# Performance work log

Hardware: AMD Instinct MI355X
Metric: run time of the kernel (lower is better)

Reference implementation:

```python
import jax, jax.numpy as jnp
import numpy as np

V = 100000   # vocab (input_size == output_size)
H = 300      # glove_embed_dim == hidden_size
L = 64       # max_length
B = 64       # batch_size


def gru_step(x, h, W_ih, W_hh, b_ih, b_hh):
    # PyTorch nn.GRU single step. x,h: [B,H]; W_*: [3H,H]; b_*: [3H]
    gi = x @ W_ih.T + b_ih
    gh = h @ W_hh.T + b_hh
    i_r, i_z, i_n = jnp.split(gi, 3, axis=-1)
    h_r, h_z, h_n = jnp.split(gh, 3, axis=-1)
    r = jax.nn.sigmoid(i_r + h_r)
    z = jax.nn.sigmoid(i_z + h_z)
    n = jnp.tanh(i_n + r * h_n)
    return (1.0 - z) * n + z * h


def setup_inputs() -> dict:
    key = jax.random.key(0)
    ks = jax.random.split(key, 12)
    s = 1.0 / np.sqrt(H)
    u = lambda k, shape: jax.random.uniform(k, shape, jnp.float32, -s, s)
    return {
        "input": jax.random.randint(ks[0], (L, B), 0, V),
        "emb": jax.random.normal(ks[1], (V, H), jnp.float32),
        "enc_W_ih": u(ks[2], (3 * H, H)), "enc_W_hh": u(ks[3], (3 * H, H)),
        "enc_b_ih": u(ks[4], (3 * H,)), "enc_b_hh": u(ks[5], (3 * H,)),
        "dec_W_ih": u(ks[6], (3 * H, H)), "dec_W_hh": u(ks[7], (3 * H, H)),
        "dec_b_ih": u(ks[8], (3 * H,)), "dec_b_hh": u(ks[9], (3 * H,)),
        "out_W": u(ks[10], (V, H)), "out_b": u(ks[11], (V,)),
    }


def reference(input, emb, enc_W_ih, enc_W_hh, enc_b_ih, enc_b_hh,
              dec_W_ih, dec_W_hh, dec_b_ih, dec_b_hh, out_W, out_b):
    max_len, batch = input.shape

    # ---- encoder: GRU over token embeddings ----
    def enc_step(h, ids):
        x = emb[ids]  # [B,H]
        h_new = gru_step(x, h, enc_W_ih, enc_W_hh, enc_b_ih, enc_b_hh)
        return h_new, None

    h0 = jnp.zeros((batch, H), jnp.float32)
    enc_h, _ = jax.lax.scan(enc_step, h0, input)

    # ---- decoder: greedy generation for max_len steps ----
    def dec_step(carry, _):
        h, ids = carry
        x = jax.nn.relu(emb[ids])
        h_new = gru_step(x, h, dec_W_ih, dec_W_hh, dec_b_ih, dec_b_hh)
        logp = jax.nn.log_softmax(h_new @ out_W.T + out_b, axis=1)  # [B,V]
        new_ids = jnp.argmax(logp, axis=1)  # topk(1)
        return (h_new, new_ids), new_ids.astype(jnp.float32)

    init_ids = jnp.zeros((batch,), jnp.int64 if input.dtype == jnp.int64 else jnp.int32)
    _, out = jax.lax.scan(dec_step, (enc_h, init_ids), None, length=max_len)
    return out  # [max_len, batch] float token ids
```

## Files before the change

kernel.cpp:

```cpp
#include <hip/hip_runtime.h>

#define HD 300
#define KC 75
#define BD 64
#define VD 100000
#define LD 64
#define NM32 3126
#define NT16 6252
#define MARGIN 0.05f

typedef unsigned long long u64;
typedef short short8 __attribute__((ext_vector_type(8)));
typedef float f32x4 __attribute__((ext_vector_type(4)));

__device__ __forceinline__ float sigm(float x) { return 1.0f / (1.0f + expf(-x)); }

__device__ __forceinline__ int tidx(int k, int b) {
  return (k >> 2) * 256 + b * 4 + (k & 3);
}

__device__ __forceinline__ unsigned enc32(float f) {
  unsigned u = __float_as_uint(f);
  return (u & 0x80000000u) ? ~u : (u | 0x80000000u);
}
__device__ __forceinline__ float dec32(unsigned e) {
  unsigned u = (e & 0x80000000u) ? (e & 0x7FFFFFFFu) : ~e;
  return __uint_as_float(u);
}
__device__ __forceinline__ unsigned short f2bf(float f) {
  unsigned u = __float_as_uint(f);
  unsigned r = u + 0x7FFFu + ((u >> 16) & 1u);
  return (unsigned short)(r >> 16);
}
__device__ __forceinline__ u64 shfl64(u64 v, int m) {
  int lo = __shfl_xor((int)(unsigned)v, m, 64);
  int hi = __shfl_xor((int)(unsigned)(v >> 32), m, 64);
  return ((u64)(unsigned)hi << 32) | (unsigned)lo;
}
__device__ __forceinline__ u64 umax64(u64 a, u64 b) { return a > b ? a : b; }
__device__ __forceinline__ void top2(u64 k, u64& b, u64& r) {
  if (k > b) { r = b; b = k; } else if (k > r) r = k;
}

__global__ __launch_bounds__(320) void k_prep(
    const int* __restrict__ input, const float* __restrict__ emb,
    float* __restrict__ xall)
{
  const int t = blockIdx.x, b = blockIdx.y;
  const int k = threadIdx.x;
  if (k >= HD) return;
  const int id = input[t * BD + b];
  xall[t * (KC * 256) + tidx(k, b)] = emb[(size_t)id * HD + k];
}

__global__ __launch_bounds__(320) void k_init(
    float* __restrict__ hT, const float* __restrict__ emb, float* __restrict__ xdec,
    unsigned* __restrict__ hbp)
{
  const int b = blockIdx.x;
  const int k = threadIdx.x;
  const int gi = b * 320 + k;
  if (gi < 10240) hbp[gi] = 0u;
  if (k >= HD) return;
  hT[tidx(k, b)] = 0.f;
  xdec[tidx(k, b)] = fmaxf(emb[k], 0.f);
}

template <bool PACK>
__global__ __launch_bounds__(768) void k_gru(
    const float* __restrict__ xT, const float* __restrict__ hT_in,
    const float* __restrict__ W_ih, const float* __restrict__ W_hh,
    const float* __restrict__ b_ih, const float* __restrict__ b_hh,
    float* __restrict__ hT_out, unsigned* __restrict__ hbp)
{
  const int w = __builtin_amdgcn_readfirstlane(threadIdx.x >> 6);
  const int b = threadIdx.x & 63;
  const int half = (w >= 6) ? 1 : 0;
  const int ww = w - 6 * half;
  const int m = ww & 1;
  const int g = ww >> 1;
  const int i0 = blockIdx.x * 4;

  const float* src = m ? hT_in : xT;
  const float* M   = m ? W_hh : W_ih;
  const float* row0 = M + (size_t)(g * HD + i0) * HD;

  float4 a0 = {0,0,0,0}, a1 = {0,0,0,0}, a2 = {0,0,0,0}, a3 = {0,0,0,0};

  const int kcB = half ? 38 : 0;
  const int kcE = half ? KC : 38;
  for (int kc = kcB; kc < kcE; kc++) {
    const float4 s = *(const float4*)(src + kc * 256 + b * 4);
    const float4 w0 = *(const float4*)(row0 + kc * 4);
    const float4 w1 = *(const float4*)(row0 + HD + kc * 4);
    const float4 w2 = *(const float4*)(row0 + 2 * HD + kc * 4);
    const float4 w3 = *(const float4*)(row0 + 3 * HD + kc * 4);
    a0.x += w0.x * s.x; a0.y += w0.y * s.y; a0.z += w0.z * s.z; a0.w += w0.w * s.w;
    a1.x += w1.x * s.x; a1.y += w1.y * s.y; a1.z += w1.z * s.z; a1.w += w1.w * s.w;
    a2.x += w2.x * s.x; a2.y += w2.y * s.y; a2.z += w2.z * s.z; a2.w += w2.w * s.w;
    a3.x += w3.x * s.x; a3.y += w3.y * s.y; a3.z += w3.z * s.z; a3.w += w3.w * s.w;
  }

  const float* bias = m ? b_hh : b_ih;
  __shared__ float sg[2][2][3][4][64];
  const float bb0 = half ? 0.f : bias[g * HD + i0 + 0];
  const float bb1 = half ? 0.f : bias[g * HD + i0 + 1];
  const float bb2 = half ? 0.f : bias[g * HD + i0 + 2];
  const float bb3 = half ? 0.f : bias[g * HD + i0 + 3];
  sg[half][m][g][0][b] = (a0.x + a0.y) + (a0.z + a0.w) + bb0;
  sg[half][m][g][1][b] = (a1.x + a1.y) + (a1.z + a1.w) + bb1;
  sg[half][m][g][2][b] = (a2.x + a2.y) + (a2.z + a2.w) + bb2;
  sg[half][m][g][3][b] = (a3.x + a3.y) + (a3.z + a3.w) + bb3;

  __shared__ float hsh[4][64];
  __syncthreads();

  if (w < 4) {
    const int r = w;
    const int i = i0 + r;
    const float xr = sg[0][0][0][r][b] + sg[1][0][0][r][b];
    const float hr = sg[0][1][0][r][b] + sg[1][1][0][r][b];
    const float xz = sg[0][0][1][r][b] + sg[1][0][1][r][b];
    const float hz = sg[0][1][1][r][b] + sg[1][1][1][r][b];
    const float xn = sg[0][0][2][r][b] + sg[1][0][2][r][b];
    const float hn = sg[0][1][2][r][b] + sg[1][1][2][r][b];
    const float rr = sigm(xr + hr);
    const float zz = sigm(xz + hz);
    const float nn = tanhf(xn + rr * hn);
    const float hp = hT_in[tidx(i, b)];
    const float h  = (1.f - zz) * nn + zz * hp;
    hT_out[tidx(i, b)] = h;
    if (PACK) hsh[r][b] = h;
  }

  if (PACK) {
    __syncthreads();
    if (w < 2) {
      const int k = i0 + 2 * w;
      const unsigned outp =
          (unsigned)f2bf(hsh[2 * w][b]) | ((unsigned)f2bf(hsh[2 * w + 1][b]) << 16);
      const int kt = k >> 5;
      const int q  = (k >> 3) & 3;
      const int p  = (k >> 1) & 3;
      const int nt = b >> 4;
      const int ln = q * 16 + (b & 15);
      hbp[((kt * 4 + nt) << 8) + ln * 4 + p] = outp;
    }
  }
}

__global__ __launch_bounds__(256) void k_pack(
    const float* __restrict__ outW, unsigned* __restrict__ Wp)
{
  const int t16 = blockIdx.x;
  const int d = threadIdx.x;
  const int lane = d >> 2, p = d & 3;
  const int v = t16 * 16 + (lane & 15);
  for (int kt = 0; kt < 10; kt++) {
    const int k = kt * 32 + (lane >> 4) * 8 + 2 * p;
    float f0 = 0.f, f1 = 0.f;
    if (v < VD) {
      if (k < HD)     f0 = outW[(size_t)v * HD + k];
      if (k + 1 < HD) f1 = outW[(size_t)v * HD + k + 1];
    }
    const unsigned out = (unsigned)f2bf(f0) | ((unsigned)f2bf(f1) << 16);
    Wp[((size_t)t16 * 10 + kt) * 256 + d] = out;
  }
}

template <bool PACKED>
__global__ __launch_bounds__(256) void k_projbf(
    const unsigned* __restrict__ Wp, const float* __restrict__ outW,
    const unsigned* __restrict__ hbp, const float* __restrict__ outb,
    u64* __restrict__ bbuf)
{
  __shared__ __align__(16) unsigned hlds[10240];

  const int w = __builtin_amdgcn_readfirstlane(threadIdx.x >> 6);
  const int lane = threadIdx.x & 63;
  const int m32 = blockIdx.x * 4 + w;
  const int m32c = (m32 < NM32) ? m32 : (NM32 - 1);
  const int t0 = m32c * 2;
  const int quad = lane >> 4;

  f32x4 acc[2][4];
#pragma unroll
  for (int mt = 0; mt < 2; mt++)
#pragma unroll
    for (int nt = 0; nt < 4; nt++) acc[mt][nt] = f32x4{0.f, 0.f, 0.f, 0.f};

  auto LOADA = [&](short8* dst, int kt) {
    if (PACKED) {
#pragma unroll
      for (int mt = 0; mt < 2; mt++)
        dst[mt] = *(const short8*)(Wp + ((size_t)(t0 + mt) * 10 + kt) * 256 + lane * 4);
    } else {
#pragma unroll
      for (int mt = 0; mt < 2; mt++) {
        const int v = (t0 + mt) * 16 + (lane & 15);
        const int kb = kt * 32 + quad * 8;
        const int vc = (v < VD) ? v : (VD - 1);
        short8 tmp;
#pragma unroll
        for (int e = 0; e < 8; e++) {
          const int kk = kb + e;
          const float f = (kk < HD && v < VD) ? outW[(size_t)vc * HD + kk] : 0.f;
          tmp[e] = (short)f2bf(f);
        }
        dst[mt] = tmp;
      }
    }
  };

  auto COMPUTE = [&](short8* a, int kt) {
#pragma unroll
    for (int nt = 0; nt < 4; nt++) {
      const short8 bf = *(const short8*)(&hlds[((kt * 4 + nt) << 8) + lane * 4]);
      acc[0][nt] = __builtin_amdgcn_mfma_f32_16x16x32_bf16(a[0], bf, acc[0][nt], 0, 0, 0);
      acc[1][nt] = __builtin_amdgcn_mfma_f32_16x16x32_bf16(a[1], bf, acc[1][nt], 0, 0, 0);
    }
  };

  short8 aA[2], aB[2];
  LOADA(aA, 0);

  {
    const uint4* hb4 = (const uint4*)hbp;
    uint4* hl4 = (uint4*)hlds;
    for (int i = threadIdx.x; i < 2560; i += 256) hl4[i] = hb4[i];
  }
  __syncthreads();
  if (m32 >= NM32) return;

#pragma unroll
  for (int kp = 0; kp < 5; kp++) {
    LOADA(aB, 2 * kp + 1);
    COMPUTE(aA, 2 * kp);
    if (kp < 4) LOADA(aA, 2 * kp + 2);
    COMPUTE(aB, 2 * kp + 1);
  }

  const int m0 = m32 * 32;
  u64 best[4], run[4];
#pragma unroll
  for (int nt = 0; nt < 4; nt++) { best[nt] = 0ull; run[nt] = 0ull; }

#pragma unroll
  for (int mt = 0; mt < 2; mt++) {
    const int vb = m0 + mt * 16 + quad * 4;
    const int vbc = (vb <= VD - 4) ? vb : (VD - 4);
    const float4 ob = *(const float4*)(outb + vbc);
#pragma unroll
    for (int nt = 0; nt < 4; nt++) {
#pragma unroll
      for (int reg = 0; reg < 4; reg++) {
        const int v = vb + reg;
        if (v < VD) {
          const float obv = (reg == 0) ? ob.x : (reg == 1) ? ob.y : (reg == 2) ? ob.z : ob.w;
          const float val = acc[mt][nt][reg] + obv;
          const u64 key = ((u64)enc32(val) << 32) | (u64)(0xFFFFFFFFu - (unsigned)v);
          top2(key, best[nt], run[nt]);
        }
      }
    }
  }

#pragma unroll
  for (int nt = 0; nt < 4; nt++) {
    u64 ob = shfl64(best[nt], 16), orr = shfl64(run[nt], 16);
    top2(ob, best[nt], run[nt]); top2(orr, best[nt], run[nt]);
    ob = shfl64(best[nt], 32); orr = shfl64(run[nt], 32);
    top2(ob, best[nt], run[nt]); top2(orr, best[nt], run[nt]);
  }

  u64 wb = best[0], wr = run[0];
  if (quad == 1) { wb = best[1]; wr = run[1]; }
  if (quad == 2) { wb = best[2]; wr = run[2]; }
  if (quad == 3) { wb = best[3]; wr = run[3]; }
  u64* dst = bbuf + (size_t)lane * (NM32 * 2) + (size_t)m32 * 2;
  dst[0] = wb; dst[1] = wr;
}

__global__ __launch_bounds__(256) void k_fin2(
    const u64* __restrict__ bbuf, const float* __restrict__ hT,
    const float* __restrict__ outW, const float* __restrict__ outb,
    const float* __restrict__ emb,
    float* __restrict__ out_row, float* __restrict__ xdec)
{
  const int b = blockIdx.x;
  const int tid = threadIdx.x;
  const int w = tid >> 6, lane = tid & 63;
  const u64* keys = bbuf + (size_t)b * (NM32 * 2);

  u64 local = 0ull;
  {
    const ulonglong2* k2 = (const ulonglong2*)keys;
    for (int i = tid; i < NM32; i += 256) {
      const ulonglong2 v = k2[i];
      local = umax64(local, umax64(v.x, v.y));
    }
  }
  for (int mm = 1; mm <= 32; mm <<= 1) local = umax64(local, shfl64(local, mm));

  __shared__ u64 wmax[4];
  __shared__ unsigned s_te;
  __shared__ int s_n;
  if (lane == 0) wmax[w] = local;
  __syncthreads();
  if (tid == 0) {
    const u64 mx = umax64(umax64(wmax[0], wmax[1]), umax64(wmax[2], wmax[3]));
    const float mv = dec32((unsigned)(mx >> 32));
    s_te = enc32(mv - MARGIN);
    s_n = 0;
  }
  __syncthreads();
  const unsigned te = s_te;

  __shared__ int cand[256];
  for (int i = tid; i < NM32 * 2; i += 256) {
    const u64 k = keys[i];
    if ((unsigned)(k >> 32) >= te && k != 0ull) {
      const int slot = atomicAdd(&s_n, 1);
      if (slot < 256) cand[slot] = (int)(0xFFFFFFFFu - (unsigned)k);
    }
  }
  __syncthreads();
  const int n = min(s_n, 256);

  u64 bk = 0ull;
  if (tid < n) {
    const int v = cand[tid];
    const float4* wr4 = (const float4*)(outW + (size_t)v * HD);
    float acc = 0.f;
    for (int c = 0; c < KC; c++) {
      const float4 wv = wr4[c];
      const float4 hv = *(const float4*)(hT + c * 256 + b * 4);
      acc += wv.x * hv.x + wv.y * hv.y + wv.z * hv.z + wv.w * hv.w;
    }
    acc += outb[v];
    bk = ((u64)enc32(acc) << 32) | (u64)(0xFFFFFFFFu - (unsigned)v);
  }
  for (int mm = 1; mm <= 32; mm <<= 1) bk = umax64(bk, shfl64(bk, mm));
  if (lane == 0) wmax[w] = bk;
  __syncthreads();

  __shared__ int s_id;
  if (tid == 0) {
    const u64 mx = umax64(umax64(wmax[0], wmax[1]), umax64(wmax[2], wmax[3]));
    const int id = (int)(0xFFFFFFFFu - (unsigned)(mx & 0xFFFFFFFFull));
    out_row[b] = (float)id;
    s_id = id;
  }
  __syncthreads();

  const int id = s_id;
  for (int k = tid; k < HD; k += 256)
    xdec[tidx(k, b)] = fmaxf(emb[(size_t)id * HD + k], 0.f);
}

extern "C" void kernel_launch(void* const* d_in, const int* in_sizes, int n_in,
                              void* d_out, int out_size, void* d_ws, size_t ws_size,
                              hipStream_t stream) {
  const int*   input  = (const int*)d_in[0];
  const float* emb    = (const float*)d_in[1];
  const float* eWih   = (const float*)d_in[2];
  const float* eWhh   = (const float*)d_in[3];
  const float* eBih   = (const float*)d_in[4];
  const float* eBhh   = (const float*)d_in[5];
  const float* dWih   = (const float*)d_in[6];
  const float* dWhh   = (const float*)d_in[7];
  const float* dBih   = (const float*)d_in[8];
  const float* dBhh   = (const float*)d_in[9];
  const float* outW   = (const float*)d_in[10];
  const float* outb   = (const float*)d_in[11];
  float* out = (float*)d_out;

  const size_t wpBytes = (size_t)NT16 * 10 * 1024;
  size_t need = wpBytes + 3201024 + 40960 + 5145600 + 6 * 256;
  const bool packed = ws_size >= need;

  size_t off = 0;
  auto take = [&](size_t nbytes) -> char* {
    char* p = (char*)d_ws + off;
    off += (nbytes + 255) & ~(size_t)255;
    return p;
  };

  unsigned* Wp = packed ? (unsigned*)take(wpBytes) : nullptr;
  u64*      bbuf = (u64*)take((size_t)BD * NM32 * 2 * 8);
  unsigned* hbp  = (unsigned*)take(40960);
  float* hA   = (float*)take(76800);
  float* hB   = (float*)take(76800);
  float* xdec = (float*)take(76800);
  float* xall = (float*)take((size_t)LD * 76800);

  if (packed) k_pack<<<NT16, 256, 0, stream>>>(outW, Wp);
  k_prep<<<dim3(LD, BD), 320, 0, stream>>>(input, emb, xall);
  k_init<<<BD, 320, 0, stream>>>(hA, emb, xdec, hbp);

  for (int t = 0; t < LD; t++) {
    float* hin  = (t & 1) ? hB : hA;
    float* hout = (t & 1) ? hA : hB;
    k_gru<false><<<75, 768, 0, stream>>>(xall + t * (KC * 256), hin,
                                         eWih, eWhh, eBih, eBhh, hout, hbp);
  }

  for (int s = 0; s < LD; s++) {
    float* hin  = (s & 1) ? hB : hA;
    float* hout = (s & 1) ? hA : hB;
    k_gru<true><<<75, 768, 0, stream>>>(xdec, hin, dWih, dWhh, dBih, dBhh, hout, hbp);
    if (packed)
      k_projbf<true><<<782, 256, 0, stream>>>(Wp, outW, hbp, outb, bbuf);
    else
      k_projbf<false><<<782, 256, 0, stream>>>(Wp, outW, hbp, outb, bbuf);
    k_fin2<<<BD, 256, 0, stream>>>(bbuf, hout, outW, outb, emb, out + s * BD, xdec);
  }
}
```

Before: 6.539 ms.

## Fuse encoder/decoder step loop into one persistent cooperative kernel with grid syncs

Replaces the ~256 per-step kernel launches (GRU, projection, finalize) with one cooperative persistent kernel of 521 blocks × 384 threads that runs all encoder and decoder steps, separated by grid-wide syncs. The aim is to remove per-launch overhead and the drain/refill gaps between dependent small kernels. The GRU block drops the K-split across 12 waves and uses 6 waves, each looping over the full K, so each wave does a longer serial dot product. The projection is regrouped to 6 waves per block so the grid covers all tiles exactly. A fallback keeps separate launches if cooperative launch is unavailable or occupancy is insufficient; grid.sync costs and the idle blocks during the GRU phases are the tradeoff.

```diff
diff --git a/kernel.cpp b/kernel.cpp
--- a/kernel.cpp
+++ b/kernel.cpp
@@ -1,4 +1,7 @@
 #include <hip/hip_runtime.h>
+#include <hip/hip_cooperative_groups.h>
+
+namespace cg = cooperative_groups;
 
 #define HD 300
 #define KC 75
@@ -8,6 +11,8 @@
 #define NM32 3126
 #define NT16 6252
 #define MARGIN 0.05f
+#define NBLK 521
+#define NTHR 384
 
 typedef unsigned long long u64;
 typedef short short8 __attribute__((ext_vector_type(8)));
@@ -42,44 +47,25 @@
   if (k > b) { r = b; b = k; } else if (k > r) r = k;
 }
 
-__global__ __launch_bounds__(320) void k_prep(
-    const int* __restrict__ input, const float* __restrict__ emb,
-    float* __restrict__ xall)
-{
-  const int t = blockIdx.x, b = blockIdx.y;
-  const int k = threadIdx.x;
-  if (k >= HD) return;
-  const int id = input[t * BD + b];
-  xall[t * (KC * 256) + tidx(k, b)] = emb[(size_t)id * HD + k];
-}
-
-__global__ __launch_bounds__(320) void k_init(
-    float* __restrict__ hT, const float* __restrict__ emb, float* __restrict__ xdec,
-    unsigned* __restrict__ hbp)
-{
-  const int b = blockIdx.x;
-  const int k = threadIdx.x;
-  const int gi = b * 320 + k;
-  if (gi < 10240) hbp[gi] = 0u;
-  if (k >= HD) return;
-  hT[tidx(k, b)] = 0.f;
-  xdec[tidx(k, b)] = fmaxf(emb[k], 0.f);
-}
-
-template <bool PACK>
-__global__ __launch_bounds__(768) void k_gru(
+union __align__(16) SM {
+  unsigned hlds[10240];
+  struct { float sg[2][3][4][64]; float hsh[4][64]; } g;
+  struct { u64 wmax[8]; int cand[256]; unsigned te; int n; int id; } f;
+};
+
+__device__ __forceinline__ void d_gru(
+    int blk, int tid,
     const float* __restrict__ xT, const float* __restrict__ hT_in,
     const float* __restrict__ W_ih, const float* __restrict__ W_hh,
     const float* __restrict__ b_ih, const float* __restrict__ b_hh,
-    float* __restrict__ hT_out, unsigned* __restrict__ hbp)
-{
-  const int w = __builtin_amdgcn_readfirstlane(threadIdx.x >> 6);
-  const int b = threadIdx.x & 63;
-  const int half = (w >= 6) ? 1 : 0;
-  const int ww = w - 6 * half;
-  const int m = ww & 1;
-  const int g = ww >> 1;
-  const int i0 = blockIdx.x * 4;
+    float* __restrict__ hT_out, unsigned* __restrict__ hbp, bool pack,
+    SM* sm)
+{
+  const int w = __builtin_amdgcn_readfirstlane(tid >> 6);
+  const int b = tid & 63;
+  const int m = w & 1;
+  const int g = w >> 1;
+  const int i0 = blk * 4;
 
   const float* src = m ? hT_in : xT;
   const float* M   = m ? W_hh : W_ih;
@@ -87,10 +73,8 @@
 
   float4 a0 = {0,0,0,0}, a1 = {0,0,0,0}, a2 = {0,0,0,0}, a3 = {0,0,0,0};
 
-  const int kcB = half ? 38 : 0;
-  const int kcE = half ? KC : 38;
-  for (int kc = kcB; kc < kcE; kc++) {
-    const float4 s = *(const float4*)(src + kc * 256 + b * 4);
+  for (int kc = 0; kc < KC; kc++) {
+    const float4 s  = *(const float4*)(src + kc * 256 + b * 4);
     const float4 w0 = *(const float4*)(row0 + kc * 4);
     const float4 w1 = *(const float4*)(row0 + HD + kc * 4);
     const float4 w2 = *(const float4*)(row0 + 2 * HD + kc * 4);
@@ -102,43 +86,30 @@
   }
 
   const float* bias = m ? b_hh : b_ih;
-  __shared__ float sg[2][2][3][4][64];
-  const float bb0 = half ? 0.f : bias[g * HD + i0 + 0];
-  const float bb1 = half ? 0.f : bias[g * HD + i0 + 1];
-  const float bb2 = half ? 0.f : bias[g * HD + i0 + 2];
-  const float bb3 = half ? 0.f : bias[g * HD + i0 + 3];
-  sg[half][m][g][0][b] = (a0.x + a0.y) + (a0.z + a0.w) + bb0;
-  sg[half][m][g][1][b] = (a1.x + a1.y) + (a1.z + a1.w) + bb1;
-  sg[half][m][g][2][b] = (a2.x + a2.y) + (a2.z + a2.w) + bb2;
-  sg[half][m][g][3][b] = (a3.x + a3.y) + (a3.z + a3.w) + bb3;
-
-  __shared__ float hsh[4][64];
+  sm->g.sg[m][g][0][b] = (a0.x + a0.y) + (a0.z + a0.w) + bias[g * HD + i0 + 0];
+  sm->g.sg[m][g][1][b] = (a1.x + a1.y) + (a1.z + a1.w) + bias[g * HD + i0 + 1];
+  sm->g.sg[m][g][2][b] = (a2.x + a2.y) + (a2.z + a2.w) + bias[g * HD + i0 + 2];
+  sm->g.sg[m][g][3][b] = (a3.x + a3.y) + (a3.z + a3.w) + bias[g * HD + i0 + 3];
   __syncthreads();
 
   if (w < 4) {
     const int r = w;
     const int i = i0 + r;
-    const float xr = sg[0][0][0][r][b] + sg[1][0][0][r][b];
-    const float hr = sg[0][1][0][r][b] + sg[1][1][0][r][b];
-    const float xz = sg[0][0][1][r][b] + sg[1][0][1][r][b];
-    const float hz = sg[0][1][1][r][b] + sg[1][1][1][r][b];
-    const float xn = sg[0][0][2][r][b] + sg[1][0][2][r][b];
-    const float hn = sg[0][1][2][r][b] + sg[1][1][2][r][b];
-    const float rr = sigm(xr + hr);
-    const float zz = sigm(xz + hz);
-    const float nn = tanhf(xn + rr * hn);
+    const float rr = sigm(sm->g.sg[0][0][r][b] + sm->g.sg[1][0][r][b]);
+    const float zz = sigm(sm->g.sg[0][1][r][b] + sm->g.sg[1][1][r][b]);
+    const float nn = tanhf(sm->g.sg[0][2][r][b] + rr * sm->g.sg[1][2][r][b]);
     const float hp = hT_in[tidx(i, b)];
     const float h  = (1.f - zz) * nn + zz * hp;
     hT_out[tidx(i, b)] = h;
-    if (PACK) hsh[r][b] = h;
-  }
-
-  if (PACK) {
+    sm->g.hsh[r][b] = h;
+  }
+
+  if (pack) {
     __syncthreads();
     if (w < 2) {
       const int k = i0 + 2 * w;
       const unsigned outp =
-          (unsigned)f2bf(hsh[2 * w][b]) | ((unsigned)f2bf(hsh[2 * w + 1][b]) << 16);
+          (unsigned)f2bf(sm->g.hsh[2 * w][b]) | ((unsigned)f2bf(sm->g.hsh[2 * w + 1][b]) << 16);
       const int kt = k >> 5;
       const int q  = (k >> 3) & 3;
       const int p  = (k >> 1) & 3;
@@ -147,6 +118,287 @@
       hbp[((kt * 4 + nt) << 8) + ln * 4 + p] = outp;
     }
   }
+}
+
+template <bool PACKED>
+__device__ __forceinline__ void d_proj(
+    int blk, int tid,
+    const unsigned* __restrict__ Wp, const float* __restrict__ outW,
+    const unsigned* __restrict__ hbp, const float* __restrict__ outb,
+    u64* __restrict__ bbuf, SM* sm)
+{
+  const int w = __builtin_amdgcn_readfirstlane(tid >> 6);
+  const int lane = tid & 63;
+  const int m32 = blk * 6 + w;
+  const int t0 = m32 * 2;
+  const int quad = lane >> 4;
+
+  f32x4 acc[2][4];
+#pragma unroll
+  for (int mt = 0; mt < 2; mt++)
+#pragma unroll
+    for (int nt = 0; nt < 4; nt++) acc[mt][nt] = f32x4{0.f, 0.f, 0.f, 0.f};
+
+  auto LOADA = [&](short8* dst, int kt) {
+    if (PACKED) {
+#pragma unroll
+      for (int mt = 0; mt < 2; mt++)
+        dst[mt] = *(const short8*)(Wp + ((size_t)(t0 + mt) * 10 + kt) * 256 + lane * 4);
+    } else {
+#pragma unroll
+      for (int mt = 0; mt < 2; mt++) {
+        const int v = (t0 + mt) * 16 + (lane & 15);
+        const int kb = kt * 32 + quad * 8;
+        const int vc = (v < VD) ? v : (VD - 1);
+        short8 tmp;
+#pragma unroll
+        for (int e = 0; e < 8; e++) {
+          const int kk = kb + e;
+          const float f = (kk < HD && v < VD) ? outW[(size_t)vc * HD + kk] : 0.f;
+          tmp[e] = (short)f2bf(f);
+        }
+        dst[mt] = tmp;
+      }
+    }
+  };
+
+  auto COMPUTE = [&](short8* a, int kt) {
+#pragma unroll
+    for (int nt = 0; nt < 4; nt++) {
+      const short8 bf = *(const short8*)(&sm->hlds[((kt * 4 + nt) << 8) + lane * 4]);
+      acc[0][nt] = __builtin_amdgcn_mfma_f32_16x16x32_bf16(a[0], bf, acc[0][nt], 0, 0, 0);
+      acc[1][nt] = __builtin_amdgcn_mfma_f32_16x16x32_bf16(a[1], bf, acc[1][nt], 0, 0, 0);
+    }
+  };
+
+  short8 aA[2], aB[2];
+  LOADA(aA, 0);
+
+  {
+    const uint4* hb4 = (const uint4*)hbp;
+    uint4* hl4 = (uint4*)sm->hlds;
+    for (int i = tid; i < 2560; i += NTHR) hl4[i] = hb4[i];
+  }
+  __syncthreads();
+
+#pragma unroll
+  for (int kp = 0; kp < 5; kp++) {
+    LOADA(aB, 2 * kp + 1);
+    COMPUTE(aA, 2 * kp);
+    if (kp < 4) LOADA(aA, 2 * kp + 2);
+    COMPUTE(aB, 2 * kp + 1);
+  }
+
+  const int m0 = m32 * 32;
+  u64 best[4], run[4];
+#pragma unroll
+  for (int nt = 0; nt < 4; nt++) { best[nt] = 0ull; run[nt] = 0ull; }
+
+#pragma unroll
+  for (int mt = 0; mt < 2; mt++) {
+    const int vb = m0 + mt * 16 + quad * 4;
+    const int vbc = (vb <= VD - 4) ? vb : (VD - 4);
+    const float4 ob = *(const float4*)(outb + vbc);
+#pragma unroll
+    for (int nt = 0; nt < 4; nt++) {
+#pragma unroll
+      for (int reg = 0; reg < 4; reg++) {
+        const int v = vb + reg;
+        if (v < VD) {
+          const float obv = (reg == 0) ? ob.x : (reg == 1) ? ob.y : (reg == 2) ? ob.z : ob.w;
+          const float val = acc[mt][nt][reg] + obv;
+          const u64 key = ((u64)enc32(val) << 32) | (u64)(0xFFFFFFFFu - (unsigned)v);
+          top2(key, best[nt], run[nt]);
+        }
+      }
+    }
+  }
+
+#pragma unroll
+  for (int nt = 0; nt < 4; nt++) {
+    u64 ob = shfl64(best[nt], 16), orr = shfl64(run[nt], 16);
+    top2(ob, best[nt], run[nt]); top2(orr, best[nt], run[nt]);
+    ob = shfl64(best[nt], 32); orr = shfl64(run[nt], 32);
+    top2(ob, best[nt], run[nt]); top2(orr, best[nt], run[nt]);
+  }
+
+  u64 wb = best[0], wr = run[0];
+  if (quad == 1) { wb = best[1]; wr = run[1]; }
+  if (quad == 2) { wb = best[2]; wr = run[2]; }
+  if (quad == 3) { wb = best[3]; wr = run[3]; }
+  u64* dst = bbuf + (size_t)lane * (NM32 * 2) + (size_t)m32 * 2;
+  dst[0] = wb; dst[1] = wr;
+}
+
+__device__ __forceinline__ void d_fin(
+    int b, int tid,
+    const u64* __restrict__ bbuf, const float* __restrict__ hT,
+    const float* __restrict__ outW, const float* __restrict__ outb,
+    const float* __restrict__ emb,
+    float* __restrict__ out_row, float* __restrict__ xdec, SM* sm)
+{
+  const int w = tid >> 6, lane = tid & 63;
+  const u64* keys = bbuf + (size_t)b * (NM32 * 2);
+
+  u64 local = 0ull;
+  {
+    const ulonglong2* k2 = (const ulonglong2*)keys;
+    for (int i = tid; i < NM32; i += NTHR) {
+      const ulonglong2 v = k2[i];
+      local = umax64(local, umax64(v.x, v.y));
+    }
+  }
+  for (int mm = 1; mm <= 32; mm <<= 1) local = umax64(local, shfl64(local, mm));
+  if (lane == 0) sm->f.wmax[w] = local;
+  __syncthreads();
+  if (tid == 0) {
+    u64 mx = 0ull;
+    for (int i = 0; i < 6; i++) mx = umax64(mx, sm->f.wmax[i]);
+    sm->f.te = enc32(dec32((unsigned)(mx >> 32)) - MARGIN);
+    sm->f.n = 0;
+  }
+  __syncthreads();
+  const unsigned te = sm->f.te;
+
+  for (int i = tid; i < NM32 * 2; i += NTHR) {
+    const u64 k = keys[i];
+    if ((unsigned)(k >> 32) >= te && k != 0ull) {
+      const int slot = atomicAdd(&sm->f.n, 1);
+      if (slot < 256) sm->f.cand[slot] = (int)(0xFFFFFFFFu - (unsigned)k);
+    }
+  }
+  __syncthreads();
+  const int n = min(sm->f.n, 256);
+
+  u64 bk = 0ull;
+  if (tid < n) {
+    const int v = sm->f.cand[tid];
+    const float4* wr4 = (const float4*)(outW + (size_t)v * HD);
+    float acc = 0.f;
+    for (int c = 0; c < KC; c++) {
+      const float4 wv = wr4[c];
+      const float4 hv = *(const float4*)(hT + c * 256 + b * 4);
+      acc += wv.x * hv.x + wv.y * hv.y + wv.z * hv.z + wv.w * hv.w;
+    }
+    acc += outb[v];
+    bk = ((u64)enc32(acc) << 32) | (u64)(0xFFFFFFFFu - (unsigned)v);
+  }
+  for (int mm = 1; mm <= 32; mm <<= 1) bk = umax64(bk, shfl64(bk, mm));
+  if (lane == 0) sm->f.wmax[w] = bk;
+  __syncthreads();
+  if (tid == 0) {
+    u64 mx = 0ull;
+    for (int i = 0; i < 6; i++) mx = umax64(mx, sm->f.wmax[i]);
+    const int id = (int)(0xFFFFFFFFu - (unsigned)(mx & 0xFFFFFFFFull));
+    out_row[b] = (float)id;
+    sm->f.id = id;
+  }
+  __syncthreads();
+
+  const int id = sm->f.id;
+  for (int k = tid; k < HD; k += NTHR)
+    xdec[tidx(k, b)] = fmaxf(emb[(size_t)id * HD + k], 0.f);
+}
+
+template <bool PACKED>
+__global__ __launch_bounds__(NTHR) void k_mega(
+    const float* __restrict__ xall, float* __restrict__ hA, float* __restrict__ hB,
+    float* __restrict__ xdec, unsigned* __restrict__ hbp, u64* __restrict__ bbuf,
+    const float* __restrict__ eWih, const float* __restrict__ eWhh,
+    const float* __restrict__ eBih, const float* __restrict__ eBhh,
+    const float* __restrict__ dWih, const float* __restrict__ dWhh,
+    const float* __restrict__ dBih, const float* __restrict__ dBhh,
+    const unsigned* __restrict__ Wp, const float* __restrict__ outW,
+    const float* __restrict__ outb, const float* __restrict__ emb,
+    float* __restrict__ out)
+{
+  __shared__ SM sm;
+  cg::grid_group grid = cg::this_grid();
+  const int blk = blockIdx.x;
+  const int tid = threadIdx.x;
+
+  for (int t = 0; t < LD; t++) {
+    const float* hin = (t & 1) ? hB : hA;
+    float* hout = (t & 1) ? hA : hB;
+    if (blk < 75)
+      d_gru(blk, tid, xall + t * (KC * 256), hin, eWih, eWhh, eBih, eBhh,
+            hout, nullptr, false, &sm);
+    __threadfence();
+    grid.sync();
+  }
+
+  for (int s = 0; s < LD; s++) {
+    const float* hin = (s & 1) ? hB : hA;
+    float* hout = (s & 1) ? hA : hB;
+    if (blk < 75)
+      d_gru(blk, tid, xdec, hin, dWih, dWhh, dBih, dBhh, hout, hbp, true, &sm);
+    __threadfence();
+    grid.sync();
+
+    d_proj<PACKED>(blk, tid, Wp, outW, hbp, outb, bbuf, &sm);
+    __threadfence();
+    grid.sync();
+
+    if (blk < BD)
+      d_fin(blk, tid, bbuf, hout, outW, outb, emb, out + s * BD, xdec, &sm);
+    __threadfence();
+    grid.sync();
+  }
+}
+
+template <bool PACK>
+__global__ __launch_bounds__(NTHR) void k_gru_g(
+    const float* __restrict__ xT, const float* __restrict__ hin,
+    const float* __restrict__ Wih, const float* __restrict__ Whh,
+    const float* __restrict__ bih, const float* __restrict__ bhh,
+    float* __restrict__ hout, unsigned* __restrict__ hbp)
+{
+  __shared__ SM sm;
+  d_gru(blockIdx.x, threadIdx.x, xT, hin, Wih, Whh, bih, bhh, hout, hbp, PACK, &sm);
+}
+
+template <bool PACKED>
+__global__ __launch_bounds__(NTHR) void k_proj_g(
+    const unsigned* __restrict__ Wp, const float* __restrict__ outW,
+    const unsigned* __restrict__ hbp, const float* __restrict__ outb,
+    u64* __restrict__ bbuf)
+{
+  __shared__ SM sm;
+  d_proj<PACKED>(blockIdx.x, threadIdx.x, Wp, outW, hbp, outb, bbuf, &sm);
+}
+
+__global__ __launch_bounds__(NTHR) void k_fin_g(
+    const u64* __restrict__ bbuf, const float* __restrict__ hT,
+    const float* __restrict__ outW, const float* __restrict__ outb,
+    const float* __restrict__ emb,
+    float* __restrict__ out_row, float* __restrict__ xdec)
+{
+  __shared__ SM sm;
+  d_fin(blockIdx.x, threadIdx.x, bbuf, hT, outW, outb, emb, out_row, xdec, &sm);
+}
+
+__global__ __launch_bounds__(320) void k_prep(
+    const int* __restrict__ input, const float* __restrict__ emb,
+    float* __restrict__ xall)
+{
+  const int t = blockIdx.x, b = blockIdx.y;
+  const int k = threadIdx.x;
+  if (k >= HD) return;
+  const int id = input[t * BD + b];
+  xall[t * (KC * 256) + tidx(k, b)] = emb[(size_t)id * HD + k];
+}
+
+__global__ __launch_bounds__(320) void k_init(
+    float* __restrict__ hT, const float* __restrict__ emb, float* __restrict__ xdec,
+    unsigned* __restrict__ hbp)
+{
+  const int b = blockIdx.x;
+  const int k = threadIdx.x;
+  const int gi = b * 320 + k;
+  if (gi < 10240) hbp[gi] = 0u;
+  if (k >= HD) return;
+  hT[tidx(k, b)] = 0.f;
+  xdec[tidx(k, b)] = fmaxf(emb[k], 0.f);
 }
 
 __global__ __launch_bounds__(256) void k_pack(
@@ -163,199 +415,9 @@
       if (k < HD)     f0 = outW[(size_t)v * HD + k];
       if (k + 1 < HD) f1 = outW[(size_t)v * HD + k + 1];
     }
-    const unsigned out = (unsigned)f2bf(f0) | ((unsigned)f2bf(f1) << 16);
-    Wp[((size_t)t16 * 10 + kt) * 256 + d] = out;
-  }
-}
-
-template <bool PACKED>
-__global__ __launch_bounds__(256) void k_projbf(
-    const unsigned* __restrict__ Wp, const float* __restrict__ outW,
-    const unsigned* __restrict__ hbp, const float* __restrict__ outb,
-    u64* __restrict__ bbuf)
-{
-  __shared__ __align__(16) unsigned hlds[10240];
-
-  const int w = __builtin_amdgcn_readfirstlane(threadIdx.x >> 6);
-  const int lane = threadIdx.x & 63;
-  const int m32 = blockIdx.x * 4 + w;
-  const int m32c = (m32 < NM32) ? m32 : (NM32 - 1);
-  const int t0 = m32c * 2;
-  const int quad = lane >> 4;
-
-  f32x4 acc[2][4];
-#pragma unroll
-  for (int mt = 0; mt < 2; mt++)
-#pragma unroll
-    for (int nt = 0; nt < 4; nt++) acc[mt][nt] = f32x4{0.f, 0.f, 0.f, 0.f};
-
-  auto LOADA = [&](short8* dst, int kt) {
-    if (PACKED) {
-#pragma unroll
-      for (int mt = 0; mt < 2; mt++)
-        dst[mt] = *(const short8*)(Wp + ((size_t)(t0 + mt) * 10 + kt) * 256 + lane * 4);
-    } else {
-#pragma unroll
-      for (int mt = 0; mt < 2; mt++) {
-        const int v = (t0 + mt) * 16 + (lane & 15);
-        const int kb = kt * 32 + quad * 8;
-        const int vc = (v < VD) ? v : (VD - 1);
-        short8 tmp;
-#pragma unroll
-        for (int e = 0; e < 8; e++) {
-          const int kk = kb + e;
-          const float f = (kk < HD && v < VD) ? outW[(size_t)vc * HD + kk] : 0.f;
-          tmp[e] = (short)f2bf(f);
-        }
-        dst[mt] = tmp;
-      }
-    }
-  };
-
-  auto COMPUTE = [&](short8* a, int kt) {
-#pragma unroll
-    for (int nt = 0; nt < 4; nt++) {
-      const short8 bf = *(const short8*)(&hlds[((kt * 4 + nt) << 8) + lane * 4]);
-      acc[0][nt] = __builtin_amdgcn_mfma_f32_16x16x32_bf16(a[0], bf, acc[0][nt], 0, 0, 0);
-      acc[1][nt] = __builtin_amdgcn_mfma_f32_16x16x32_bf16(a[1], bf, acc[1][nt], 0, 0, 0);
-    }
-  };
-
-  short8 aA[2], aB[2];
-  LOADA(aA, 0);
-
-  {
-    const uint4* hb4 = (const uint4*)hbp;
-    uint4* hl4 = (uint4*)hlds;
-    for (int i = threadIdx.x; i < 2560; i += 256) hl4[i] = hb4[i];
-  }
-  __syncthreads();
-  if (m32 >= NM32) return;
-
-#pragma unroll
-  for (int kp = 0; kp < 5; kp++) {
-    LOADA(aB, 2 * kp + 1);
-    COMPUTE(aA, 2 * kp);
-    if (kp < 4) LOADA(aA, 2 * kp + 2);
-    COMPUTE(aB, 2 * kp + 1);
-  }
-
-  const int m0 = m32 * 32;
-  u64 best[4], run[4];
-#pragma unroll
-  for (int nt = 0; nt < 4; nt++) { best[nt] = 0ull; run[nt] = 0ull; }
-
-#pragma unroll
-  for (int mt = 0; mt < 2; mt++) {
-    const int vb = m0 + mt * 16 + quad * 4;
-    const int vbc = (vb <= VD - 4) ? vb : (VD - 4);
-    const float4 ob = *(const float4*)(outb + vbc);
-#pragma unroll
-    for (int nt = 0; nt < 4; nt++) {
-#pragma unroll
-      for (int reg = 0; reg < 4; reg++) {
-        const int v = vb + reg;
-        if (v < VD) {
-          const float obv = (reg == 0) ? ob.x : (reg == 1) ? ob.y : (reg == 2) ? ob.z : ob.w;
-          const float val = acc[mt][nt][reg] + obv;
-          const u64 key = ((u64)enc32(val) << 32) | (u64)(0xFFFFFFFFu - (unsigned)v);
-          top2(key, best[nt], run[nt]);
-        }
-      }
-    }
-  }
-
-#pragma unroll
-  for (int nt = 0; nt < 4; nt++) {
-    u64 ob = shfl64(best[nt], 16), orr = shfl64(run[nt], 16);
-    top2(ob, best[nt], run[nt]); top2(orr, best[nt], run[nt]);
-    ob = shfl64(best[nt], 32); orr = shfl64(run[nt], 32);
-    top2(ob, best[nt], run[nt]); top2(orr, best[nt], run[nt]);
-  }
-
-  u64 wb = best[0], wr = run[0];
-  if (quad == 1) { wb = best[1]; wr = run[1]; }
-  if (quad == 2) { wb = best[2]; wr = run[2]; }
-  if (quad == 3) { wb = best[3]; wr = run[3]; }
-  u64* dst = bbuf + (size_t)lane * (NM32 * 2) + (size_t)m32 * 2;
-  dst[0] = wb; dst[1] = wr;
-}
-
-__global__ __launch_bounds__(256) void k_fin2(
-    const u64* __restrict__ bbuf, const float* __restrict__ hT,
-    const float* __restrict__ outW, const float* __restrict__ outb,
-    const float* __restrict__ emb,
-    float* __restrict__ out_row, float* __restrict__ xdec)
-{
-  const int b = blockIdx.x;
-  const int tid = threadIdx.x;
-  const int w = tid >> 6, lane = tid & 63;
-  const u64* keys = bbuf + (size_t)b * (NM32 * 2);
-
-  u64 local = 0ull;
-  {
-    const ulonglong2* k2 = (const ulonglong2*)keys;
-    for (int i = tid; i < NM32; i += 256) {
-      const ulonglong2 v = k2[i];
-      local = umax64(local, umax64(v.x, v.y));
-    }
-  }
-  for (int mm = 1; mm <= 32; mm <<= 1) local = umax64(local, shfl64(local, mm));
-
-  __shared__ u64 wmax[4];
-  __shared__ unsigned s_te;
-  __shared__ int s_n;
-  if (lane == 0) wmax[w] = local;
-  __syncthreads();
-  if (tid == 0) {
-    const u64 mx = umax64(umax64(wmax[0], wmax[1]), umax64(wmax[2], wmax[3]));
-    const float mv = dec32((unsigned)(mx >> 32));
-    s_te = enc32(mv - MARGIN);
-    s_n = 0;
-  }
-  __syncthreads();
-  const unsigned te = s_te;
-
-  __shared__ int cand[256];
-  for (int i = tid; i < NM32 * 2; i += 256) {
-    const u64 k = keys[i];
-    if ((unsigned)(k >> 32) >= te && k != 0ull) {
-      const int slot = atomicAdd(&s_n, 1);
-      if (slot < 256) cand[slot] = (int)(0xFFFFFFFFu - (unsigned)k);
-    }
-  }
-  __syncthreads();
-  const int n = min(s_n, 256);
-
-  u64 bk = 0ull;
-  if (tid < n) {
-    const int v = cand[tid];
-    const float4* wr4 = (const float4*)(outW + (size_t)v * HD);
-    float acc = 0.f;
-    for (int c = 0; c < KC; c++) {
-      const float4 wv = wr4[c];
-      const float4 hv = *(const float4*)(hT + c * 256 + b * 4);
-      acc += wv.x * hv.x + wv.y * hv.y + wv.z * hv.z + wv.w * hv.w;
-    }
-    acc += outb[v];
-    bk = ((u64)enc32(acc) << 32) | (u64)(0xFFFFFFFFu - (unsigned)v);
-  }
-  for (int mm = 1; mm <= 32; mm <<= 1) bk = umax64(bk, shfl64(bk, mm));
-  if (lane == 0) wmax[w] = bk;
-  __syncthreads();
-
-  __shared__ int s_id;
-  if (tid == 0) {
-    const u64 mx = umax64(umax64(wmax[0], wmax[1]), umax64(wmax[2], wmax[3]));
-    const int id = (int)(0xFFFFFFFFu - (unsigned)(mx & 0xFFFFFFFFull));
-    out_row[b] = (float)id;
-    s_id = id;
-  }
-  __syncthreads();
-
-  const int id = s_id;
-  for (int k = tid; k < HD; k += 256)
-    xdec[tidx(k, b)] = fmaxf(emb[(size_t)id * HD + k], 0.f);
+    const unsigned outp = (unsigned)f2bf(f0) | ((unsigned)f2bf(f1) << 16);
+    Wp[((size_t)t16 * 10 + kt) * 256 + d] = outp;
+  }
 }
 
 extern "C" void kernel_launch(void* const* d_in, const int* in_sizes, int n_in,
@@ -394,25 +456,63 @@
   float* xdec = (float*)take(76800);
   float* xall = (float*)take((size_t)LD * 76800);
 
+  using MegaFn = void (*)(const float*, float*, float*, float*, unsigned*, u64*,
+                          const float*, const float*, const float*, const float*,
+                          const float*, const float*, const float*, const float*,
+                          const unsigned*, const float*, const float*, const float*,
+                          float*);
+
+  static int s_mega = -2;
+  if (s_mega == -2) {
+    s_mega = 0;
+    int coop = 0;
+    if (hipDeviceGetAttribute(&coop, hipDeviceAttributeCooperativeLaunch, 0) == hipSuccess && coop) {
+      int ncu = 0;
+      hipDeviceGetAttribute(&ncu, hipDeviceAttributeMultiprocessorCount, 0);
+      int occ = 0;
+      MegaFn fp = k_mega<true>;
+      if (hipOccupancyMaxActiveBlocksPerMultiprocessor(
+              &occ, reinterpret_cast<const void*>(fp), NTHR, 0) == hipSuccess &&
+          occ * ncu >= NBLK)
+        s_mega = 1;
+    }
+  }
+
   if (packed) k_pack<<<NT16, 256, 0, stream>>>(outW, Wp);
   k_prep<<<dim3(LD, BD), 320, 0, stream>>>(input, emb, xall);
   k_init<<<BD, 320, 0, stream>>>(hA, emb, xdec, hbp);
 
-  for (int t = 0; t < LD; t++) {
-    float* hin  = (t & 1) ? hB : hA;
-    float* hout = (t & 1) ? hA : hB;
-    k_gru<false><<<75, 768, 0, stream>>>(xall + t * (KC * 256), hin,
-                                         eWih, eWhh, eBih, eBhh, hout, hbp);
-  }
-
-  for (int s = 0; s < LD; s++) {
-    float* hin  = (s & 1) ? hB : hA;
-    float* hout = (s & 1) ? hA : hB;
-    k_gru<true><<<75, 768, 0, stream>>>(xdec, hin, dWih, dWhh, dBih, dBhh, hout, hbp);
-    if (packed)
-      k_projbf<true><<<782, 256, 0, stream>>>(Wp, outW, hbp, outb, bbuf);
-    else
-      k_projbf<false><<<782, 256, 0, stream>>>(Wp, outW, hbp, outb, bbuf);
-    k_fin2<<<BD, 256, 0, stream>>>(bbuf, hout, outW, outb, emb, out + s * BD, xdec);
-  }
-}
+  bool done = false;
+  if (s_mega == 1) {
+    const float* xall_c = xall;
+    const unsigned* Wp_c = Wp;
+    void* args[19] = {
+      (void*)&xall_c, (void*)&hA, (void*)&hB, (void*)&xdec, (void*)&hbp, (void*)&bbuf,
+      (void*)&eWih, (void*)&eWhh, (void*)&eBih, (void*)&eBhh,
+      (void*)&dWih, (void*)&dWhh, (void*)&dBih, (void*)&dBhh,
+      (void*)&Wp_c, (void*)&outW, (void*)&outb, (void*)&emb, (void*)&out };
+    MegaFn fn = packed ? (MegaFn)k_mega<true> : (MegaFn)k_mega<false>;
+    hipError_t e = hipLaunchCooperativeKernel(
+        reinterpret_cast<const void*>(fn), dim3(NBLK), dim3(NTHR), args, 0, stream);
+    done = (e == hipSuccess);
+  }
+
+  if (!done) {
+    for (int t = 0; t < LD; t++) {
+      float* hin  = (t & 1) ? hB : hA;
+      float* hout = (t & 1) ? hA : hB;
+      k_gru_g<false><<<75, NTHR, 0, stream>>>(xall + t * (KC * 256), hin,
+                                              eWih, eWhh, eBih, eBhh, hout, hbp);
+    }
+    for (int s = 0; s < LD; s++) {
+      float* hin  = (s & 1) ? hB : hA;
+      float* hout = (s & 1) ? hA : hB;
+      k_gru_g<true><<<75, NTHR, 0, stream>>>(xdec, hin, dWih, dWhh, dBih, dBhh, hout, hbp);
+      if (packed)
+        k_proj_g<true><<<NBLK, NTHR, 0, stream>>>(Wp, outW, hbp, outb, bbuf);
+      else
+        k_proj_g<false><<<NBLK, NTHR, 0, stream>>>(Wp, outW, hbp, outb, bbuf);
+      k_fin_g<<<BD, NTHR, 0, stream>>>(bbuf, hout, outW, outb, emb, out + s * BD, xdec);
+    }
+  }
+}
```

Measured after the change: 6.059 ms. 7.3% less time.
